# Kernel tuning notes

Measured on AMD Instinct MI355X. Metric: run time of the kernel, lower is better.

## Reference

```python
import jax, jax.numpy as jnp
import numpy as np
import itertools

_CODESZ = 8

_NORM12 = np.array([[3,1,1,1,3,3,3,3],[1,3,1,1,3,3,3,3],[1,1,3,1,3,3,3,3],[1,1,1,3,3,3,3,3],[3,3,3,1,3,3,1,1],[3,3,3,1,3,1,3,1],[3,3,3,1,1,3,3,1],[3,3,3,1,3,1,1,3],[3,3,3,1,1,3,1,3],[3,3,3,1,1,1,3,3],[3,3,1,3,3,3,1,1],[3,3,1,3,3,1,3,1],[3,3,1,3,1,3,3,1],[3,3,1,3,3,1,1,3],[3,3,1,3,1,3,1,3],[3,3,1,3,1,1,3,3],[3,1,3,3,3,3,1,1],[3,1,3,3,3,1,3,1],[3,1,3,3,1,3,3,1],[3,1,3,3,3,1,1,3],[3,1,3,3,1,3,1,3],[1,3,3,3,1,1,3,3],[1,3,3,3,3,3,1,1],[1,3,3,3,3,1,3,1],[1,3,3,3,1,3,3,1],[1,3,3,3,3,1,1,3],[1,3,3,3,1,3,1,3],[1,3,3,3,1,1,3,3],[3,3,1,1,3,3,3,1]], dtype=np.float32) / 2.0


def build_grid_abs():
    # unique |v| for v in (Z+1/2)^8 with even sum and ||v||^2 <= 10 -> coords in {.5,1.5,2.5},
    # lexicographically sorted (matches torch.unique(dim=0) ordering) -> 227 rows, +29 norm-12 rows = 256
    rows = [v for v in itertools.product((0.5, 1.5, 2.5), repeat=8) if sum(c * c for c in v) <= 10.0]
    grid = np.concatenate([np.array(rows, dtype=np.float32), _NORM12], axis=0)
    even = (np.round(grid.sum(-1)).astype(np.int64) % 2 == 0)
    return grid.astype(np.float16), even


def _fwht(x):
    # unnormalized Sylvester-order fast Walsh-Hadamard transform along last axis (power of 2)
    shape = x.shape
    L = shape[-1]
    y = x.reshape(-1, L)
    c = 1
    while c < L:
        y = y.reshape(-1, L // (2 * c), 2, c)
        a, b = y[:, :, 0, :], y[:, :, 1, :]
        y = jnp.stack([a + b, a - b], axis=2).reshape(-1, L)
        c *= 2
    return y.reshape(shape)


def matmul_hadU(X, hadK, K):
    # equals quip-sharp matmul_hadU: FWHT on length-(n/K) blocks, then hadK across blocks, / sqrt(n)
    n = X.shape[-1]
    x = _fwht(X.reshape(-1, K, n // K))
    if K > 1:
        x = jnp.einsum('kl,blc->bkc', hadK.astype(x.dtype), x)
    return x.reshape(*X.shape[:-1], n) * np.float32(1.0 / np.sqrt(n))


def matmul_hadUt(X, hadK, K):
    return matmul_hadU(X, hadK.T, K)


def decompress_e8p(Qidxs, grid_abs, grid_abs_even):
    # 16-bit code: [15:8] abs-grid index, [7:1] sign flips for dims 1..7, [0] +/- 1/4 shift.
    # dim-0 sign is inferred so the total flip count parity keeps the point on the E8 lattice.
    q = Qidxs.astype(jnp.int32)
    abs_idx = (q >> 8) & 0xFF                                   # [m, n]
    sign_bits = (q >> 1) & 0x7F
    shift_bit = q & 1
    bits = (sign_bits[..., None] >> jnp.arange(7, dtype=jnp.int32)) & 1  # [m, n, 7]
    parity = bits.sum(-1) & 1
    abs_odd = 1 - grid_abs_even[abs_idx].astype(jnp.int32)
    sign0 = parity ^ abs_odd
    neg = jnp.concatenate([sign0[..., None], bits], axis=-1)    # [m, n, 8]
    w_abs = grid_abs[abs_idx]                                   # [m, n, 8] fp16
    signs = (1 - 2 * neg).astype(w_abs.dtype)
    shift = jnp.where(shift_bit, 0.25, -0.25).astype(w_abs.dtype)[..., None]
    w = w_abs * signs + shift
    return w.reshape(q.shape[0], -1)                            # [m, n*8]


def setup_inputs() -> dict:
    key = jax.random.key(0)
    k1, k2, k3, k4 = jax.random.split(key, 4)
    m, n_codes, tokens = 4096, 512, 2048
    in_f = n_codes * _CODESZ
    grid, even = build_grid_abs()
    return {
        'input': jax.random.normal(k1, (tokens, in_f), jnp.float32),
        'Qidxs': jax.random.randint(k2, (m, n_codes), 0, 65536, jnp.int32),
        'SU': jnp.sign(jax.random.normal(k3, (in_f,), jnp.float32)),
        'SV': jnp.sign(jax.random.normal(k4, (m,), jnp.float32)),
        'Wscale': jnp.full((1,), 0.95, jnp.float32),
        'had_left': jnp.ones((1, 1), jnp.float32),
        'had_right': jnp.ones((1, 1), jnp.float32),
        'K_left': 1,
        'K_right': 1,
        'grid_abs': jnp.asarray(grid),
        'grid_abs_even': jnp.asarray(even),
    }


def reference(input, Qidxs, SU, SV, Wscale, had_left, had_right, K_left, K_right, grid_abs, grid_abs_even):
    m, n_codes = Qidxs.shape
    x = input.reshape(-1, n_codes * _CODESZ).astype(jnp.float32)
    x = x * SU
    x = matmul_hadUt(x, had_left, K_left)
    W = decompress_e8p(Qidxs, grid_abs, grid_abs_even)          # [m, n*8] fp16
    x = (x.astype(jnp.float16) @ W.T).astype(jnp.float32)       # [tokens, m]
    x = x * Wscale
    x = matmul_hadU(x, had_right, K_right)
    x = x * SV
    return x.reshape(*input.shape[:-1], m)
```

## Files before the change

### kernel.cpp

```cpp
#include <hip/hip_runtime.h>

typedef short s16;
typedef unsigned short us16;
typedef signed char i8;
typedef __attribute__((ext_vector_type(8))) short s16x8;
typedef __attribute__((ext_vector_type(8))) unsigned short u16x8;
typedef __attribute__((ext_vector_type(8))) signed char i8x8;
typedef __attribute__((ext_vector_type(16))) signed char i8x16;
typedef __attribute__((ext_vector_type(4))) int i32x4;

#define TOKENS 2048
#define INF    4096
#define OUTF   4096
#define GK     4096

__device__ __forceinline__ us16 f2bf(float f) {
    union { float f; unsigned u; } v; v.f = f;
    unsigned r = v.u + 0x7FFFu + ((v.u >> 16) & 1u);
    return (us16)(r >> 16);
}
__device__ __forceinline__ float bf2f(us16 u) {
    unsigned x = ((unsigned)u) << 16;
    float f; __builtin_memcpy(&f, &x, 4);
    return f;
}

__device__ __forceinline__ void fwht16(float v[16]) {
#pragma unroll
    for (int s = 1; s < 16; s <<= 1)
#pragma unroll
        for (int j = 0; j < 16; ++j)
            if (!(j & s)) {
                float a = v[j], b = v[j + s];
                v[j]     = a + b;
                v[j + s] = a - b;
            }
}

__global__ __launch_bounds__(256) void k_pre(const float* __restrict__ X,
                                             const float* __restrict__ SU,
                                             i8* __restrict__ Y,
                                             float* __restrict__ ZS,
                                             const int* __restrict__ Q,
                                             const void* __restrict__ gridraw,
                                             i8* __restrict__ W) {
    __shared__ float s[4096 + 272];
    const int tid = threadIdx.x;

    if (blockIdx.x < TOKENS) {
        const int row = blockIdx.x;
        const int hi = tid >> 4, lo = tid & 15;
        float v[16];
        const float* xr = X + (size_t)row * INF;

#pragma unroll
        for (int j = 0; j < 16; ++j) v[j] = xr[j * 256 + tid] * SU[j * 256 + tid];
        fwht16(v);
#pragma unroll
        for (int j = 0; j < 16; ++j) s[272 * j + 17 * hi + lo] = v[j];
        __syncthreads();

#pragma unroll
        for (int j = 0; j < 16; ++j) v[j] = s[272 * hi + 17 * j + lo];
        fwht16(v);
#pragma unroll
        for (int j = 0; j < 16; ++j) s[272 * hi + 17 * j + lo] = v[j];
        __syncthreads();

        const int base = 272 * hi + 17 * lo;
#pragma unroll
        for (int j = 0; j < 16; ++j) v[j] = s[base + j];
        fwht16(v);

        float m16 = 0.f;
#pragma unroll
        for (int j = 0; j < 16; ++j) m16 = fmaxf(m16, fabsf(v[j]));
        __syncthreads();
        s[tid] = m16;
        __syncthreads();
#pragma unroll
        for (int off = 128; off > 0; off >>= 1) {
            if (tid < off) s[tid] = fmaxf(s[tid], s[tid + off]);
            __syncthreads();
        }
        const float vmax = fmaxf(s[0], 1e-30f);
        const float qs = 127.0f / vmax;

        i8x16 o;
#pragma unroll
        for (int j = 0; j < 16; ++j) o[j] = (i8)__float2int_rn(v[j] * qs);
        *reinterpret_cast<i8x16*>(Y + (size_t)row * INF + tid * 16) = o;
        if (tid == 0) ZS[row] = vmax * (0.015625f / 508.0f);
    } else {
        float (*gT)[256] = (float(*)[256])s;
        int* gOdd = (int*)(s + 2048);

        const unsigned short* gu = (const unsigned short*)gridraw;
        const float*          gf = (const float*)gridraw;
        const unsigned short  p0 = gu[0];

        float sum = 0.f;
#pragma unroll
        for (int j = 0; j < 8; ++j) {
            float v;
            if (p0 == 0x3800) {
                unsigned short u = gu[tid * 8 + j];
                _Float16 hv; __builtin_memcpy(&hv, &u, 2);
                v = (float)hv;
            } else if (p0 == 0x3F00) {
                v = bf2f(gu[tid * 8 + j]);
            } else {
                v = gf[tid * 8 + j];
            }
            gT[j][tid] = v;
            sum += v;
        }
        gOdd[tid] = ((int)(sum + 0.5f)) & 1;
        __syncthreads();

        const int chunk0 = (blockIdx.x - TOKENS) * 8;
#pragma unroll
        for (int c = 0; c < 8; ++c) {
            const int code = (chunk0 + c) * 256 + tid;
            const int q        = Q[code];
            const int absIdx   = (q >> 8) & 255;
            const int signBits = (q >> 1) & 127;
            const float shift  = (q & 1) ? 1.0f : -1.0f;
            const int neg0 = (__popc(signBits) ^ gOdd[absIdx]) & 1;

            i8x8 o;
            o[0] = (i8)__float2int_rn(gT[0][absIdx] * 4.0f * (1.0f - 2.0f * (float)neg0) + shift);
#pragma unroll
            for (int i = 1; i < 8; ++i) {
                float sg = 1.0f - 2.0f * (float)((signBits >> (i - 1)) & 1);
                o[i] = (i8)__float2int_rn(gT[i][absIdx] * 4.0f * sg + shift);
            }
            *reinterpret_cast<i8x8*>(W + (size_t)code * 8) = o;
        }
    }
}

#define BM 128
#define BN 256
#define BK 64

__global__ __launch_bounds__(512, 4) void k_gemm(const i8* __restrict__ A,
                                                 const i8* __restrict__ B,
                                                 const float* __restrict__ ZS,
                                                 us16* __restrict__ Z0,
                                                 us16* __restrict__ Z1) {
    __shared__ __align__(16) i8 lA[2][BM * BK];
    __shared__ __align__(16) i8 lB[2][BN * BK];
    const int tid  = threadIdx.x;
    const int lane = tid & 63;
    const int w    = tid >> 6;
    const int wr   = w >> 2, wc = w & 3;
    const int laneRow = lane & 15, laneK = lane >> 4;

    const int bid = blockIdx.x;
    const int swz = (bid & 7) * 64 + (bid >> 3);
    const int ks  = swz >> 8;
    const int rem = swz & 255;
    const int mT  = rem >> 4;
    const int nT  = rem & 15;
    const int KT  = (GK / 2) / BK;
    const size_t kbase = (size_t)ks * (GK / 2);

    us16* __restrict__ Z = (ks == 1) ? Z1 : Z0;

    size_t aOff;
    {
        int rr = tid >> 2, cc = tid & 3;
        int sc = cc ^ ((rr >> 1) & 3);
        aOff = (size_t)(mT * BM + rr) * GK + kbase + sc * 16;
    }
    const int ldsOffA = w * 64 * 16;
    size_t bOff[2];
    int ldsOffB[2];
#pragma unroll
    for (int j = 0; j < 2; ++j) {
        int ch = j * 512 + tid;
        int rr = ch >> 2, cc = ch & 3;
        int sc = cc ^ ((rr >> 1) & 3);
        bOff[j] = (size_t)(nT * BN + rr) * GK + kbase + sc * 16;
        ldsOffB[j] = (j * 512 + w * 64) * 16;
    }

    int aB[4], aX[4], bB[4], bX[4];
#pragma unroll
    for (int mi = 0; mi < 4; ++mi) {
        int r = wr * 64 + mi * 16 + laneRow;
        aB[mi] = r * 64; aX[mi] = (r >> 1) & 3;
    }
#pragma unroll
    for (int nj = 0; nj < 4; ++nj) {
        int r = wc * 64 + nj * 16 + laneRow;
        bB[nj] = r * 64; bX[nj] = (r >> 1) & 3;
    }

    i32x4 acc[4][4] = {};

#define STAGE(t, buf) do { const size_t _ko = (size_t)(t) * BK; \
    __builtin_amdgcn_global_load_lds( \
        (const __attribute__((address_space(1))) void*)(A + aOff + _ko), \
        (__attribute__((address_space(3))) void*)(&lA[buf][0] + ldsOffA), 16, 0, 0); \
    _Pragma("unroll") \
    for (int j = 0; j < 2; ++j) \
        __builtin_amdgcn_global_load_lds( \
            (const __attribute__((address_space(1))) void*)(B + bOff[j] + _ko), \
            (__attribute__((address_space(3))) void*)(&lB[buf][0] + ldsOffB[j]), 16, 0, 0); \
    } while (0)

    STAGE(0, 0);
    STAGE(1, 1);
    asm volatile("s_waitcnt vmcnt(3)" ::: "memory");
    __builtin_amdgcn_sched_barrier(0);
    __builtin_amdgcn_s_barrier();

    int cur = 0;
    for (int t = 0; t < KT; ++t) {
        const i8* pA = &lA[cur][0];
        const i8* pB = &lB[cur][0];

        i32x4 af[4], bf[4];
#pragma unroll
        for (int mi = 0; mi < 4; ++mi)
            af[mi] = *reinterpret_cast<const i32x4*>(pA + aB[mi] + (laneK ^ aX[mi]) * 16);
#pragma unroll
        for (int nj = 0; nj < 4; ++nj)
            bf[nj] = *reinterpret_cast<const i32x4*>(pB + bB[nj] + (laneK ^ bX[nj]) * 16);

        asm volatile("s_waitcnt lgkmcnt(0)" ::: "memory");
        __builtin_amdgcn_sched_barrier(0);
        __builtin_amdgcn_s_barrier();

        if (t + 2 < KT) { STAGE(t + 2, cur); }

#pragma unroll
        for (int mi = 0; mi < 4; ++mi)
#pragma unroll
            for (int nj = 0; nj < 4; ++nj)
                acc[mi][nj] = __builtin_amdgcn_mfma_i32_16x16x64_i8(
                    af[mi], bf[nj], acc[mi][nj], 0, 0, 0);

        if (t + 1 < KT) {
            if (t + 2 < KT) {
                asm volatile("s_waitcnt vmcnt(3)" ::: "memory");
            } else {
                asm volatile("s_waitcnt vmcnt(0)" ::: "memory");
            }
            __builtin_amdgcn_sched_barrier(0);
            __builtin_amdgcn_s_barrier();
        }
        cur ^= 1;
    }
#undef STAGE

    const int colB = nT * BN + wc * 64 + laneRow;
    const int rowB = mT * BM + wr * 64 + laneK * 4;
#pragma unroll
    for (int mi = 0; mi < 4; ++mi) {
#pragma unroll
        for (int rg = 0; rg < 4; ++rg) {
            const int row = rowB + mi * 16 + rg;
            const float zs = ZS[row];
#pragma unroll
            for (int nj = 0; nj < 4; ++nj)
                Z[(size_t)row * OUTF + colB + nj * 16]
                    = f2bf((float)acc[mi][nj][rg] * zs);
        }
    }
}

__global__ __launch_bounds__(256) void k_out(const us16* __restrict__ Z0,
                                             const us16* __restrict__ Z1,
                                             float* __restrict__ OUT,
                                             const float* __restrict__ SV,
                                             const float* __restrict__ wscale) {
    __shared__ float s[4096 + 272];
    const int row = blockIdx.x, t = threadIdx.x;
    float v[16];
    const us16* zr0 = Z0 + (size_t)row * OUTF;
    const us16* zr1 = Z1 + (size_t)row * OUTF;

    {
        u16x8 a0 = reinterpret_cast<const u16x8*>(zr0 + t * 16)[0];
        u16x8 a1 = reinterpret_cast<const u16x8*>(zr0 + t * 16)[1];
        u16x8 b0 = reinterpret_cast<const u16x8*>(zr1 + t * 16)[0];
        u16x8 b1 = reinterpret_cast<const u16x8*>(zr1 + t * 16)[1];
#pragma unroll
        for (int j = 0; j < 8; ++j) {
            v[j]     = bf2f(a0[j]) + bf2f(b0[j]);
            v[j + 8] = bf2f(a1[j]) + bf2f(b1[j]);
        }
    }
    fwht16(v);
#pragma unroll
    for (int j = 0; j < 16; ++j) s[17 * t + j] = v[j];
    __syncthreads();

    const int pa = 272 * (t >> 4) + (t & 15);
#pragma unroll
    for (int j = 0; j < 16; ++j) v[j] = s[pa + 17 * j];
    fwht16(v);
#pragma unroll
    for (int j = 0; j < 16; ++j) s[pa + 17 * j] = v[j];
    __syncthreads();

    const int pb = 17 * (t >> 4) + (t & 15);
#pragma unroll
    for (int j = 0; j < 16; ++j) v[j] = s[272 * j + pb];
    fwht16(v);

    const float sc = wscale[0] * 0.015625f;
    float* orow = OUT + (size_t)row * OUTF;
#pragma unroll
    for (int j = 0; j < 16; ++j)
        orow[j * 256 + t] = v[j] * sc * SV[j * 256 + t];
}

extern "C" void kernel_launch(void* const* d_in, const int* in_sizes, int n_in,
                              void* d_out, int out_size, void* d_ws, size_t ws_size,
                              hipStream_t stream) {
    const float* input  = (const float*)d_in[0];
    const int*   Qidxs  = (const int*)d_in[1];
    const float* SU     = (const float*)d_in[2];
    const float* SV     = (const float*)d_in[3];
    const float* Wscale = (const float*)d_in[4];
    const void*  grid   = (const void*)d_in[9];

    i8*    W  = (i8*)d_ws;
    i8*    Y  = (i8*)((char*)d_ws + (size_t)16 * 1024 * 1024);
    us16*  Z0 = (us16*)((char*)d_ws + (size_t)24 * 1024 * 1024);
    us16*  Z1 = (us16*)((char*)d_ws + (size_t)40 * 1024 * 1024);
    float* ZS = (float*)((char*)d_ws + (size_t)56 * 1024 * 1024);

    hipLaunchKernelGGL(k_pre, dim3(TOKENS + 1024), dim3(256), 0, stream,
                       input, SU, Y, ZS, Qidxs, grid, W);
    hipLaunchKernelGGL(k_gemm, dim3(512), dim3(512), 0, stream,
                       Y, W, ZS, Z0, Z1);
    hipLaunchKernelGGL(k_out, dim3(TOKENS), dim3(256), 0, stream,
                       Z0, Z1, (float*)d_out, SV, Wscale);
}
```

Before: 73.68 us.

## Load GEMM A operand directly from global into registers, bypassing LDS

Drops the LDS staging buffer for the A tile. Each wave now reads its A fragments straight from global memory into registers, prefetching the next K-step while the current one feeds the MFMAs. B staging is simplified so a load is issued every iteration (clamped to the last tile), which gives a uniform vmcnt wait. This cuts LDS traffic and shared memory use, but the four column-waves that share the same A rows now each fetch them from global/L2. The per-lane 16-byte row-strided loads are also less coalesced.

```diff
diff --git a/kernel.cpp b/kernel.cpp
--- a/kernel.cpp
+++ b/kernel.cpp
@@ -149,7 +149,6 @@
                                                  const float* __restrict__ ZS,
                                                  us16* __restrict__ Z0,
                                                  us16* __restrict__ Z1) {
-    __shared__ __align__(16) i8 lA[2][BM * BK];
     __shared__ __align__(16) i8 lB[2][BN * BK];
     const int tid  = threadIdx.x;
     const int lane = tid & 63;
@@ -168,13 +167,13 @@
 
     us16* __restrict__ Z = (ks == 1) ? Z1 : Z0;
 
-    size_t aOff;
-    {
-        int rr = tid >> 2, cc = tid & 3;
-        int sc = cc ^ ((rr >> 1) & 3);
-        aOff = (size_t)(mT * BM + rr) * GK + kbase + sc * 16;
-    }
-    const int ldsOffA = w * 64 * 16;
+    const i8* ap[4];
+#pragma unroll
+    for (int mi = 0; mi < 4; ++mi) {
+        int r = mT * BM + wr * 64 + mi * 16 + laneRow;
+        ap[mi] = A + (size_t)r * GK + kbase + (size_t)laneK * 16;
+    }
+
     size_t bOff[2];
     int ldsOffB[2];
 #pragma unroll
@@ -186,12 +185,7 @@
         ldsOffB[j] = (j * 512 + w * 64) * 16;
     }
 
-    int aB[4], aX[4], bB[4], bX[4];
-#pragma unroll
-    for (int mi = 0; mi < 4; ++mi) {
-        int r = wr * 64 + mi * 16 + laneRow;
-        aB[mi] = r * 64; aX[mi] = (r >> 1) & 3;
-    }
+    int bB[4], bX[4];
 #pragma unroll
     for (int nj = 0; nj < 4; ++nj) {
         int r = wc * 64 + nj * 16 + laneRow;
@@ -200,10 +194,7 @@
 
     i32x4 acc[4][4] = {};
 
-#define STAGE(t, buf) do { const size_t _ko = (size_t)(t) * BK; \
-    __builtin_amdgcn_global_load_lds( \
-        (const __attribute__((address_space(1))) void*)(A + aOff + _ko), \
-        (__attribute__((address_space(3))) void*)(&lA[buf][0] + ldsOffA), 16, 0, 0); \
+#define STAGE_B(t, buf) do { const size_t _ko = (size_t)(t) * BK; \
     _Pragma("unroll") \
     for (int j = 0; j < 2; ++j) \
         __builtin_amdgcn_global_load_lds( \
@@ -211,21 +202,26 @@
             (__attribute__((address_space(3))) void*)(&lB[buf][0] + ldsOffB[j]), 16, 0, 0); \
     } while (0)
 
-    STAGE(0, 0);
-    STAGE(1, 1);
-    asm volatile("s_waitcnt vmcnt(3)" ::: "memory");
+    i32x4 afc[4], afn[4];
+#pragma unroll
+    for (int mi = 0; mi < 4; ++mi)
+        afc[mi] = *reinterpret_cast<const i32x4*>(ap[mi]);
+    STAGE_B(0, 0);
+    STAGE_B(1, 1);
+    asm volatile("s_waitcnt vmcnt(2)" ::: "memory");
     __builtin_amdgcn_sched_barrier(0);
     __builtin_amdgcn_s_barrier();
 
     int cur = 0;
     for (int t = 0; t < KT; ++t) {
-        const i8* pA = &lA[cur][0];
         const i8* pB = &lB[cur][0];
 
-        i32x4 af[4], bf[4];
+        const size_t an = (size_t)((t + 1 < KT) ? (t + 1) : (KT - 1)) * BK;
 #pragma unroll
         for (int mi = 0; mi < 4; ++mi)
-            af[mi] = *reinterpret_cast<const i32x4*>(pA + aB[mi] + (laneK ^ aX[mi]) * 16);
+            afn[mi] = *reinterpret_cast<const i32x4*>(ap[mi] + an);
+
+        i32x4 bf[4];
 #pragma unroll
         for (int nj = 0; nj < 4; ++nj)
             bf[nj] = *reinterpret_cast<const i32x4*>(pB + bB[nj] + (laneK ^ bX[nj]) * 16);
@@ -234,27 +230,25 @@
         __builtin_amdgcn_sched_barrier(0);
         __builtin_amdgcn_s_barrier();
 
-        if (t + 2 < KT) { STAGE(t + 2, cur); }
+        STAGE_B((size_t)((t + 2 < KT) ? (t + 2) : (KT - 1)), cur);
 
 #pragma unroll
         for (int mi = 0; mi < 4; ++mi)
 #pragma unroll
             for (int nj = 0; nj < 4; ++nj)
                 acc[mi][nj] = __builtin_amdgcn_mfma_i32_16x16x64_i8(
-                    af[mi], bf[nj], acc[mi][nj], 0, 0, 0);
+                    afc[mi], bf[nj], acc[mi][nj], 0, 0, 0);
 
         if (t + 1 < KT) {
-            if (t + 2 < KT) {
-                asm volatile("s_waitcnt vmcnt(3)" ::: "memory");
-            } else {
-                asm volatile("s_waitcnt vmcnt(0)" ::: "memory");
-            }
+            asm volatile("s_waitcnt vmcnt(2)" ::: "memory");
             __builtin_amdgcn_sched_barrier(0);
             __builtin_amdgcn_s_barrier();
         }
+#pragma unroll
+        for (int mi = 0; mi < 4; ++mi) afc[mi] = afn[mi];
         cur ^= 1;
     }
-#undef STAGE
+#undef STAGE_B
 
     const int colB = nT * BN + wc * 64 + laneRow;
     const int rowB = mT * BM + wr * 64 + laneK * 4;
```

Result: slower. 109.0 us (+47.9%).
